# Performance work log

Measured on AMD Instinct MI355X. Metric: run time of the kernel, lower is better.

The kernel has to match this reference:

```python
import jax, jax.numpy as jnp
import numpy as np

B, P, ED, AD, DD, E, V, T = 64, 196, 2048, 512, 512, 300, 1000, 96


def setup_inputs() -> dict:
    key = jax.random.key(0)
    ks = jax.random.split(key, 24)
    s = 0.02  # small init scale for weights
    lens = jax.random.randint(ks[2], (B,), 2, T + 1).astype(jnp.int32)
    lens = lens.at[0].set(T)  # ensure max(decode_lengths) == T-1 (static)
    return {
        'encoder_out': jax.random.normal(ks[0], (B, P, ED), jnp.float32),
        'encoded_captions': jax.random.randint(ks[1], (B, T), 0, V),
        'caption_lengths': lens,
        'emb': jax.random.uniform(ks[3], (V, E), jnp.float32, -0.1, 0.1),
        'W_enc_att': jax.random.normal(ks[4], (ED, AD), jnp.float32) * s,
        'b_enc_att': jnp.zeros((AD,), jnp.float32),
        'W_dec_att': jax.random.normal(ks[5], (DD, AD), jnp.float32) * s,
        'b_dec_att': jnp.zeros((AD,), jnp.float32),
        'w_full': jax.random.normal(ks[6], (AD,), jnp.float32) * s,
        'b_full': jnp.zeros((), jnp.float32),
        'W_init_h': jax.random.normal(ks[7], (ED, DD), jnp.float32) * s,
        'b_init_h': jnp.zeros((DD,), jnp.float32),
        'W_init_c': jax.random.normal(ks[8], (ED, DD), jnp.float32) * s,
        'b_init_c': jnp.zeros((DD,), jnp.float32),
        'W_fbeta': jax.random.normal(ks[9], (DD, ED), jnp.float32) * s,
        'b_fbeta': jnp.zeros((ED,), jnp.float32),
        'W_ih': jax.random.normal(ks[10], (E + ED, 4 * DD), jnp.float32) * s,
        'b_ih': jnp.zeros((4 * DD,), jnp.float32),
        'W_hh': jax.random.normal(ks[11], (DD, 4 * DD), jnp.float32) * s,
        'b_hh': jnp.zeros((4 * DD,), jnp.float32),
        'W_fc': jax.random.uniform(ks[12], (DD, V), jnp.float32, -0.1, 0.1),
        'b_fc': jnp.zeros((V,), jnp.float32),
    }


def reference(encoder_out, encoded_captions, caption_lengths, emb,
              W_enc_att, b_enc_att, W_dec_att, b_dec_att, w_full, b_full,
              W_init_h, b_init_h, W_init_c, b_init_c, W_fbeta, b_fbeta,
              W_ih, b_ih, W_hh, b_hh, W_fc, b_fc):
    # Sort by caption length, descending (stable like torch.sort on ints)
    sort_ind = jnp.argsort(-caption_lengths)
    lens = caption_lengths[sort_ind]
    eo = encoder_out[sort_ind]                  # [B,P,ED]
    caps = encoded_captions[sort_ind]           # [B,T]
    decode_lengths = lens - 1                   # [B]

    embs = emb[caps]                            # [B,T,E]
    mean_eo = eo.mean(axis=1)                   # [B,ED]
    h0 = mean_eo @ W_init_h + b_init_h          # [B,DD]
    c0 = mean_eo @ W_init_c + b_init_c

    # encoder-side attention projection is step-invariant: hoist it
    att1 = eo @ W_enc_att + b_enc_att           # [B,P,AD]

    Tdec = T - 1
    ts = jnp.arange(Tdec)
    masks = (decode_lengths[None, :] > ts[:, None]).astype(eo.dtype)  # [Tdec,B]
    emb_seq = jnp.swapaxes(embs[:, :Tdec, :], 0, 1)                    # [Tdec,B,E]

    def step(carry, xs):
        h, c = carry
        emb_t, m = xs                           # [B,E], [B]
        mb = m[:, None]
        # Bahdanau attention
        att2 = h @ W_dec_att + b_dec_att        # [B,AD]
        e = jnp.einsum('bpa,a->bp', jax.nn.relu(att1 + att2[:, None, :]), w_full) + b_full
        alpha = jax.nn.softmax(e, axis=1)       # [B,P]
        awe = jnp.einsum('bpd,bp->bd', eo, alpha)  # [B,ED]
        gate = jax.nn.sigmoid(h @ W_fbeta + b_fbeta)
        x = jnp.concatenate([emb_t, gate * awe], axis=1)  # [B,E+ED]
        # LSTMCell (torch gate order: i, f, g, o)
        gates = x @ W_ih + b_ih + h @ W_hh + b_hh
        i, f, g, o = jnp.split(gates, 4, axis=1)
        c_new = jax.nn.sigmoid(f) * c + jax.nn.sigmoid(i) * jnp.tanh(g)
        h_new = jax.nn.sigmoid(o) * jnp.tanh(c_new)
        # only active rows (sorted so they are a prefix) update state
        h2 = mb * h_new + (1.0 - mb) * h
        c2 = mb * c_new + (1.0 - mb) * c
        preds = (h2 @ W_fc + b_fc) * mb         # dropout = identity (eval)
        return (h2, c2), (preds, alpha * mb)

    (_, _), (preds, alphas) = jax.lax.scan(step, (h0, c0), (emb_seq, masks))
    predictions = jnp.swapaxes(preds, 0, 1)     # [B,Tdec,V]
    alphas = jnp.swapaxes(alphas, 0, 1)         # [B,Tdec,P]
    return predictions, caps, decode_lengths, alphas, sort_ind
```

## Files before the change

### kernel.cpp

```cpp
#include <hip/hip_runtime.h>
#include <stddef.h>
#include <math.h>

static constexpr int B = 64, P = 196, ED = 2048, AD = 512, DD = 512, E = 300, V = 1000, T = 96, TD = 95;
static constexpr int KX = E + ED;
static constexpr int KTOT = KX + DD;
static constexpr int KSPLIT = 8;
static constexpr int KPER = 368;
static constexpr int NG = 4 * DD;

static constexpr size_t POFF   = 0;
static constexpr size_t CAPOFF = (size_t)B * TD * V;
static constexpr size_t DLOFF  = CAPOFF + (size_t)B * T;
static constexpr size_t AOFF   = DLOFF + B;
static constexpr size_t SOFF   = AOFF + (size_t)B * TD * P;

__device__ __forceinline__ float sigm(float x) { return 1.0f / (1.0f + expf(-x)); }

__global__ __launch_bounds__(64) void k_sort(const int* __restrict__ lens,
                                             const int* __restrict__ caps_in,
                                             int* __restrict__ sidx,
                                             int* __restrict__ dlen,
                                             int* __restrict__ caps_s,
                                             unsigned int* __restrict__ cnt,
                                             float* __restrict__ out) {
    __shared__ int sl[B];
    __shared__ int ss[B];
    int i = threadIdx.x;
    sl[i] = lens[i];
    cnt[i] = 0u;
    __syncthreads();
    int li = sl[i];
    int r = 0;
    for (int j = 0; j < B; j++) {
        int lj = sl[j];
        r += (lj > li) || (lj == li && j < i);
    }
    ss[r] = i;
    sidx[r] = i;
    dlen[r] = li - 1;
    out[DLOFF + r] = (float)(li - 1);
    out[SOFF + r] = (float)i;
    __syncthreads();
    for (int idx = i; idx < B * T; idx += B) {
        int b = idx / T, tt = idx % T;
        int v = caps_in[ss[b] * T + tt];
        caps_s[idx] = v;
        out[CAPOFF + idx] = (float)v;
    }
}

__global__ __launch_bounds__(256) void k_emball(const float* __restrict__ emb,
                                                const int* __restrict__ caps_s,
                                                float* __restrict__ embT) {
    int t = blockIdx.x;
    int k0 = blockIdx.y * 60;
    for (int l = threadIdx.x; l < 60 * 64; l += 256) {
        int r = l >> 6, b = l & 63;
        int k = k0 + r;
        int cap = caps_s[b * T + t];
        embT[((size_t)t * E + k) * B + b] = emb[(size_t)cap * E + k];
    }
}

__global__ __launch_bounds__(256) void k_mean(const float* __restrict__ eo,
                                              const int* __restrict__ sidx,
                                              float* __restrict__ mean_eo) {
    int b = blockIdx.y;
    int d = blockIdx.x * 256 + threadIdx.x;
    const float* base = eo + ((size_t)sidx[b] * P) * ED + d;
    float s = 0.f;
    for (int p = 0; p < P; p++) s += base[(size_t)p * ED];
    mean_eo[(size_t)b * ED + d] = s * (1.0f / (float)P);
}

__global__ __launch_bounds__(256) void k_init(const float* __restrict__ mean_eo,
                                              const float* __restrict__ Wh, const float* __restrict__ bh,
                                              const float* __restrict__ Wc, const float* __restrict__ bc,
                                              float* __restrict__ h0, float* __restrict__ c0,
                                              float* __restrict__ xT) {
    int idx = blockIdx.x * 256 + threadIdx.x;
    int b = idx >> 9, j = idx & 511;
    const float* m = mean_eo + (size_t)b * ED;
    float ah = bh[j], ac = bc[j];
    for (int k = 0; k < ED; k++) {
        float mv = m[k];
        ah += mv * Wh[(size_t)k * DD + j];
        ac += mv * Wc[(size_t)k * DD + j];
    }
    h0[idx] = ah;
    c0[idx] = ac;
    xT[(size_t)(KX + DD + j) * B + b] = ah;
}

__global__ __launch_bounds__(256) void k_att1(const float* __restrict__ eo,
                                              const float* __restrict__ W,
                                              const float* __restrict__ bias,
                                              const int* __restrict__ sidx,
                                              float* __restrict__ att1) {
    int m0 = blockIdx.x * 64, n0 = blockIdx.y * 64;
    __shared__ float sA[16][68];
    __shared__ float sB[16][68];
    int tid = threadIdx.x;
    int tx = tid & 15, ty = tid >> 4;
    float acc[4][4] = {};

    int la_m = tid >> 2;
    int la_k = (tid & 3) * 4;
    int lb_k = tid >> 4;
    int lb_n = (tid & 15) * 4;

    int mA = m0 + la_m;
    int bA = mA / P, pA = mA % P;
    const float* arow = eo + ((size_t)sidx[bA] * P + pA) * ED;

    for (int k0 = 0; k0 < ED; k0 += 16) {
        float4 av = *(const float4*)(arow + k0 + la_k);
        sA[la_k + 0][la_m] = av.x;
        sA[la_k + 1][la_m] = av.y;
        sA[la_k + 2][la_m] = av.z;
        sA[la_k + 3][la_m] = av.w;
        float4 bv = *(const float4*)(W + (size_t)(k0 + lb_k) * AD + n0 + lb_n);
        *(float4*)&sB[lb_k][lb_n] = bv;
        __syncthreads();
#pragma unroll
        for (int kk = 0; kk < 16; kk++) {
            float4 a4 = *(const float4*)&sA[kk][ty * 4];
            float4 b4 = *(const float4*)&sB[kk][tx * 4];
            float av_[4] = {a4.x, a4.y, a4.z, a4.w};
            float bv_[4] = {b4.x, b4.y, b4.z, b4.w};
#pragma unroll
            for (int i = 0; i < 4; i++)
#pragma unroll
                for (int j = 0; j < 4; j++) acc[i][j] += av_[i] * bv_[j];
        }
        __syncthreads();
    }
#pragma unroll
    for (int i = 0; i < 4; i++) {
        int m = m0 + ty * 4 + i;
        int n = n0 + tx * 4;
        float4 o;
        o.x = acc[i][0] + bias[n + 0];
        o.y = acc[i][1] + bias[n + 1];
        o.z = acc[i][2] + bias[n + 2];
        o.w = acc[i][3] + bias[n + 3];
        *(float4*)(att1 + (size_t)m * AD + n) = o;
    }
}

__global__ __launch_bounds__(256) void kA1(const float* __restrict__ hprev,
                                           const float* __restrict__ Wda, const float* __restrict__ bda,
                                           const float* __restrict__ Wfb, const float* __restrict__ bfb,
                                           float* __restrict__ att2g,
                                           float* __restrict__ fg) {
    int bx = blockIdx.x;
    int tid = threadIdx.x;
    int n0 = bx * 32;
    bool is_att = (n0 < AD);
    const float* W = is_att ? Wda : Wfb;
    int ld = is_att ? AD : ED;
    int colb = is_att ? n0 : n0 - AD;
    __shared__ float sH[2][16][68];
    __shared__ float sW[2][16][36];
    float acc[4][2] = {};
    int tb = tid & 15, tn = tid >> 4;
    int hb = tid >> 2, hq = tid & 3;
    int wk = tid >> 3, wn = (tid & 7) * 4;

    float4 hreg = *(const float4*)(hprev + (size_t)hb * DD + hq * 4);
    float4 wreg = make_float4(0.f, 0.f, 0.f, 0.f);
    if (tid < 128) wreg = *(const float4*)(W + (size_t)wk * ld + colb + wn);
    sH[0][hq * 4 + 0][hb] = hreg.x;
    sH[0][hq * 4 + 1][hb] = hreg.y;
    sH[0][hq * 4 + 2][hb] = hreg.z;
    sH[0][hq * 4 + 3][hb] = hreg.w;
    if (tid < 128) *(float4*)&sW[0][wk][wn] = wreg;
    __syncthreads();

    for (int tl = 0; tl < 32; tl++) {
        int cur = tl & 1, nxt = cur ^ 1;
        if (tl < 31) {
            int k0 = (tl + 1) * 16;
            hreg = *(const float4*)(hprev + (size_t)hb * DD + k0 + hq * 4);
            if (tid < 128) wreg = *(const float4*)(W + (size_t)(k0 + wk) * ld + colb + wn);
        }
#pragma unroll
        for (int kk = 0; kk < 16; kk++) {
            float4 hv = *(const float4*)&sH[cur][kk][tb * 4];
            float w0 = sW[cur][kk][tn * 2 + 0];
            float w1 = sW[cur][kk][tn * 2 + 1];
            acc[0][0] += hv.x * w0; acc[0][1] += hv.x * w1;
            acc[1][0] += hv.y * w0; acc[1][1] += hv.y * w1;
            acc[2][0] += hv.z * w0; acc[2][1] += hv.z * w1;
            acc[3][0] += hv.w * w0; acc[3][1] += hv.w * w1;
        }
        if (tl < 31) {
            sH[nxt][hq * 4 + 0][hb] = hreg.x;
            sH[nxt][hq * 4 + 1][hb] = hreg.y;
            sH[nxt][hq * 4 + 2][hb] = hreg.z;
            sH[nxt][hq * 4 + 3][hb] = hreg.w;
            if (tid < 128) *(float4*)&sW[nxt][wk][wn] = wreg;
        }
        __syncthreads();
    }
#pragma unroll
    for (int i = 0; i < 4; i++)
#pragma unroll
        for (int j = 0; j < 2; j++) {
            int b = tb * 4 + i;
            int n = n0 + tn * 2 + j;
            float v = acc[i][j];
            if (is_att) att2g[(size_t)b * AD + n] = v + bda[n];
            else {
                int d = n - AD;
                fg[(size_t)b * ED + d] = sigm(v + bfb[d]);
            }
        }
}

__global__ __launch_bounds__(1024) void kA2(const float* __restrict__ att2g,
                                            const float* __restrict__ att1,
                                            const float* __restrict__ wf,
                                            const float* __restrict__ bfv,
                                            const int* __restrict__ dlen,
                                            float* __restrict__ alpha,
                                            float* __restrict__ out, int t) {
    int b = blockIdx.x;
    int tid = threadIdx.x;
    __shared__ float sa2[AD];
    __shared__ float swf[AD];
    __shared__ float se[P];
    __shared__ float red[1024];

    if (tid < AD) {
        sa2[tid] = att2g[(size_t)b * AD + tid];
        swf[tid] = wf[tid];
    }
    __syncthreads();

    int w = tid >> 6, lane = tid & 63;
    float bf0 = bfv[0];
#pragma unroll 2
    for (int p = w; p < P; p += 16) {
        const float* row = att1 + ((size_t)b * P + p) * AD + lane * 8;
        float4 u0 = *(const float4*)row;
        float4 u1 = *(const float4*)(row + 4);
        float4 s0 = *(const float4*)&sa2[lane * 8];
        float4 s1 = *(const float4*)&sa2[lane * 8 + 4];
        float4 w0 = *(const float4*)&swf[lane * 8];
        float4 w1 = *(const float4*)&swf[lane * 8 + 4];
        float acc = fmaxf(u0.x + s0.x, 0.f) * w0.x + fmaxf(u0.y + s0.y, 0.f) * w0.y +
                    fmaxf(u0.z + s0.z, 0.f) * w0.z + fmaxf(u0.w + s0.w, 0.f) * w0.w +
                    fmaxf(u1.x + s1.x, 0.f) * w1.x + fmaxf(u1.y + s1.y, 0.f) * w1.y +
                    fmaxf(u1.z + s1.z, 0.f) * w1.z + fmaxf(u1.w + s1.w, 0.f) * w1.w;
#pragma unroll
        for (int m = 32; m >= 1; m >>= 1) acc += __shfl_xor(acc, m, 64);
        if (lane == 0) se[p] = acc + bf0;
    }
    __syncthreads();

    red[tid] = (tid < P) ? se[tid] : -1e30f;
    __syncthreads();
    for (int s = 512; s > 0; s >>= 1) {
        if (tid < s) red[tid] = fmaxf(red[tid], red[tid + s]);
        __syncthreads();
    }
    float mx = red[0];
    __syncthreads();
    float ex = (tid < P) ? expf(se[tid] - mx) : 0.f;
    red[tid] = ex;
    __syncthreads();
    for (int s = 512; s > 0; s >>= 1) {
        if (tid < s) red[tid] += red[tid + s];
        __syncthreads();
    }
    float inv = 1.0f / red[0];
    if (tid < P) {
        float a = ex * inv;
        alpha[(size_t)b * P + tid] = a;
        float m = (dlen[b] > t) ? 1.f : 0.f;
        out[AOFF + ((size_t)b * TD + t) * P + tid] = a * m;
    }
}

__global__ __launch_bounds__(256) void kB(const float* __restrict__ eo,
                                          const int* __restrict__ sidx,
                                          const float* __restrict__ alpha,
                                          const float* __restrict__ fg,
                                          float* __restrict__ xT) {
    int b = blockIdx.y, ch = blockIdx.x, tid = threadIdx.x;
    int pg = tid >> 6, lane = tid & 63;
    __shared__ float sal[P];
    __shared__ float part[4][260];
    if (tid < P) sal[tid] = alpha[(size_t)b * P + tid];
    __syncthreads();
    int d = ch * 256 + lane * 4;
    const float* base = eo + ((size_t)sidx[b] * P) * ED + d;
    float ax = 0.f, ay = 0.f, az = 0.f, aw = 0.f;
#pragma unroll 7
    for (int i = 0; i < 49; i++) {
        int p = pg + i * 4;
        float4 v = *(const float4*)(base + (size_t)p * ED);
        float a = sal[p];
        ax += v.x * a; ay += v.y * a; az += v.z * a; aw += v.w * a;
    }
    part[pg][lane * 4 + 0] = ax;
    part[pg][lane * 4 + 1] = ay;
    part[pg][lane * 4 + 2] = az;
    part[pg][lane * 4 + 3] = aw;
    __syncthreads();
    if (tid < 64) {
        int d0 = ch * 256 + tid * 4;
        float4 g = *(const float4*)(fg + (size_t)b * ED + d0);
        float s0 = part[0][tid * 4 + 0] + part[1][tid * 4 + 0] + part[2][tid * 4 + 0] + part[3][tid * 4 + 0];
        float s1 = part[0][tid * 4 + 1] + part[1][tid * 4 + 1] + part[2][tid * 4 + 1] + part[3][tid * 4 + 1];
        float s2 = part[0][tid * 4 + 2] + part[1][tid * 4 + 2] + part[2][tid * 4 + 2] + part[3][tid * 4 + 2];
        float s3 = part[0][tid * 4 + 3] + part[1][tid * 4 + 3] + part[2][tid * 4 + 3] + part[3][tid * 4 + 3];
        xT[(size_t)(E + d0 + 0) * B + b] = g.x * s0;
        xT[(size_t)(E + d0 + 1) * B + b] = g.y * s1;
        xT[(size_t)(E + d0 + 2) * B + b] = g.z * s2;
        xT[(size_t)(E + d0 + 3) * B + b] = g.w * s3;
    }
}

__global__ __launch_bounds__(256) void kCD(const float* __restrict__ xT,
                                           const float* __restrict__ embT_t,
                                           const float* __restrict__ xh_r,
                                           const float* __restrict__ Wih,
                                           const float* __restrict__ Whh,
                                           float* __restrict__ part,
                                           unsigned int* __restrict__ cnt,
                                           const float* __restrict__ bih,
                                           const float* __restrict__ bhh,
                                           const float* __restrict__ h0,
                                           float* __restrict__ hseq,
                                           const float* __restrict__ cread,
                                           float* __restrict__ cwrite,
                                           const int* __restrict__ dlen,
                                           float* __restrict__ xh_w, int t) {
    int bx = blockIdx.x;
    int ks = bx >> 6, nb = bx & 63;
    int n0 = nb * 32;
    int tid = threadIdx.x;
    int tb = tid & 15, tn = tid >> 4;
    int wk = tid >> 3, wn = (tid & 7) * 4;
    __shared__ float sW[2][16][36];
    __shared__ unsigned int sOld;
    float acc[4][2] = {};
    int kbase = ks * KPER;

    auto ldw = [&](int tile) -> float4 {
        int kg = kbase + tile * 16 + wk;
        float4 wv = make_float4(0.f, 0.f, 0.f, 0.f);
        if (kg < KX) wv = *(const float4*)&Wih[(size_t)kg * NG + n0 + wn];
        else if (kg < KTOT) wv = *(const float4*)&Whh[(size_t)(kg - KX) * NG + n0 + wn];
        return wv;
    };

    float4 wreg = make_float4(0.f, 0.f, 0.f, 0.f);
    if (tid < 128) {
        wreg = ldw(0);
        *(float4*)&sW[0][wk][wn] = wreg;
    }
    __syncthreads();

    for (int tile = 0; tile < 23; tile++) {
        int cur = tile & 1, nxt = cur ^ 1;
        if (tile < 22 && tid < 128) wreg = ldw(tile + 1);
#pragma unroll
        for (int kk = 0; kk < 16; kk++) {
            int kg = kbase + tile * 16 + kk;
            float4 xv = make_float4(0.f, 0.f, 0.f, 0.f);
            if (kg < E) xv = *(const float4*)&embT_t[(size_t)kg * B + tb * 4];
            else if (kg < KX) xv = *(const float4*)&xT[(size_t)kg * B + tb * 4];
            else if (kg < KTOT) xv = *(const float4*)&xh_r[(size_t)(kg - KX) * B + tb * 4];
            float w0 = sW[cur][kk][tn * 2 + 0];
            float w1 = sW[cur][kk][tn * 2 + 1];
            acc[0][0] += xv.x * w0; acc[0][1] += xv.x * w1;
            acc[1][0] += xv.y * w0; acc[1][1] += xv.y * w1;
            acc[2][0] += xv.z * w0; acc[2][1] += xv.z * w1;
            acc[3][0] += xv.w * w0; acc[3][1] += xv.w * w1;
        }
        if (tile < 22 && tid < 128) *(float4*)&sW[nxt][wk][wn] = wreg;
        __syncthreads();
    }

#pragma unroll
    for (int i = 0; i < 4; i++)
#pragma unroll
        for (int j = 0; j < 2; j++) {
            int b = tb * 4 + i, lc = tn * 2 + j;
            __hip_atomic_store(&part[((size_t)ks * B + b) * NG + n0 + lc], acc[i][j],
                               __ATOMIC_RELAXED, __HIP_MEMORY_SCOPE_AGENT);
        }
    __syncthreads();
    int jg = nb & 15;
    if (tid == 0)
        sOld = __hip_atomic_fetch_add(&cnt[jg], 1u, __ATOMIC_ACQ_REL, __HIP_MEMORY_SCOPE_AGENT);
    __syncthreads();
    if (sOld != 31u) return;

    if (tid == 0)
        __hip_atomic_store(&cnt[jg], 0u, __ATOMIC_RELAXED, __HIP_MEMORY_SCOPE_AGENT);

    const float* holds = (t == 0) ? h0 : (hseq + (size_t)(t - 1) * B * DD);
#pragma unroll
    for (int rep = 0; rep < 8; rep++) {
        int idx = rep * 256 + tid;
        int bb = idx >> 5;
        int jj = idx & 31;
        int j = jg * 32 + jj;
        float g4[4];
#pragma unroll
        for (int g = 0; g < 4; g++) {
            float gv = bih[g * DD + j] + bhh[g * DD + j];
#pragma unroll
            for (int s = 0; s < KSPLIT; s++)
                gv += __hip_atomic_load(&part[((size_t)s * B + bb) * NG + g * 512 + j],
                                        __ATOMIC_RELAXED, __HIP_MEMORY_SCOPE_AGENT);
            g4[g] = gv;
        }
        float cold = cread[(size_t)bb * DD + j];
        float hold = holds[(size_t)bb * DD + j];
        float cnew = sigm(g4[1]) * cold + sigm(g4[0]) * tanhf(g4[2]);
        float hnew = sigm(g4[3]) * tanhf(cnew);
        bool m = dlen[bb] > t;
        float h2 = m ? hnew : hold;
        float c2 = m ? cnew : cold;
        hseq[(size_t)t * B * DD + (size_t)bb * DD + j] = h2;
        cwrite[(size_t)bb * DD + j] = c2;
        xh_w[(size_t)j * B + bb] = h2;
    }
}

__global__ __launch_bounds__(256) void k_predsall(const float* __restrict__ hseq,
                                                  const float* __restrict__ Wfc,
                                                  const float* __restrict__ bfc,
                                                  const int* __restrict__ dlen,
                                                  float* __restrict__ out) {
    int t = blockIdx.x;
    int n0 = blockIdx.y * 64;
    int tid = threadIdx.x;
    int tx = tid & 15, ty = tid >> 4;
    __shared__ float sA[16][68];
    __shared__ float sB[16][68];
    float acc[4][4] = {};
    const float* A = hseq + (size_t)t * B * DD;

    for (int k0 = 0; k0 < DD; k0 += 16) {
        {
            int b = tid >> 2, q = tid & 3;
            float4 hv = *(const float4*)(A + (size_t)b * DD + k0 + q * 4);
            sA[q * 4 + 0][b] = hv.x;
            sA[q * 4 + 1][b] = hv.y;
            sA[q * 4 + 2][b] = hv.z;
            sA[q * 4 + 3][b] = hv.w;
        }
        {
            int kk = tid >> 4, nn = (tid & 15) * 4;
            int c = n0 + nn;
            const float* wrow = Wfc + (size_t)(k0 + kk) * V;
            float4 wv;
            if (c + 3 < V) wv = *(const float4*)(wrow + c);
            else {
                wv.x = (c + 0 < V) ? wrow[c + 0] : 0.f;
                wv.y = (c + 1 < V) ? wrow[c + 1] : 0.f;
                wv.z = (c + 2 < V) ? wrow[c + 2] : 0.f;
                wv.w = (c + 3 < V) ? wrow[c + 3] : 0.f;
            }
            *(float4*)&sB[kk][nn] = wv;
        }
        __syncthreads();
#pragma unroll
        for (int kk = 0; kk < 16; kk++) {
            float4 a4 = *(const float4*)&sA[kk][ty * 4];
            float4 b4 = *(const float4*)&sB[kk][tx * 4];
            float av_[4] = {a4.x, a4.y, a4.z, a4.w};
            float bv_[4] = {b4.x, b4.y, b4.z, b4.w};
#pragma unroll
            for (int i = 0; i < 4; i++)
#pragma unroll
                for (int j = 0; j < 4; j++) acc[i][j] += av_[i] * bv_[j];
        }
        __syncthreads();
    }
#pragma unroll
    for (int i = 0; i < 4; i++) {
        int b = ty * 4 + i;
        bool m = dlen[b] > t;
#pragma unroll
        for (int j = 0; j < 4; j++) {
            int n = n0 + tx * 4 + j;
            if (n < V)
                out[POFF + ((size_t)b * TD + t) * V + n] = m ? (acc[i][j] + bfc[n]) : 0.f;
        }
    }
}

extern "C" void kernel_launch(void* const* d_in, const int* in_sizes, int n_in,
                              void* d_out, int out_size, void* d_ws, size_t ws_size,
                              hipStream_t stream) {
    const float* eo    = (const float*)d_in[0];
    const int*   caps  = (const int*)d_in[1];
    const int*   lens  = (const int*)d_in[2];
    const float* emb   = (const float*)d_in[3];
    const float* Wea   = (const float*)d_in[4];
    const float* bea   = (const float*)d_in[5];
    const float* Wda   = (const float*)d_in[6];
    const float* bda   = (const float*)d_in[7];
    const float* wfull = (const float*)d_in[8];
    const float* bfull = (const float*)d_in[9];
    const float* Wih_  = (const float*)d_in[10];
    const float* bih_  = (const float*)d_in[11];
    const float* Wic   = (const float*)d_in[12];
    const float* bic   = (const float*)d_in[13];
    const float* Wfb   = (const float*)d_in[14];
    const float* bfb   = (const float*)d_in[15];
    const float* Wih   = (const float*)d_in[16];
    const float* bih   = (const float*)d_in[17];
    const float* Whh   = (const float*)d_in[18];
    const float* bhh   = (const float*)d_in[19];
    const float* Wfc   = (const float*)d_in[20];
    const float* bfc   = (const float*)d_in[21];
    float* out = (float*)d_out;

    char* w = (char*)d_ws;
    auto carve = [&](size_t bytes) -> void* {
        void* p = (void*)w;
        w += (bytes + 255) & ~(size_t)255;
        return p;
    };
    int* sidx      = (int*)carve(B * 4);
    int* dlen      = (int*)carve(B * 4);
    int* caps_s    = (int*)carve((size_t)B * T * 4);
    unsigned int* cnt = (unsigned int*)carve(64 * 4);
    float* mean_eo = (float*)carve((size_t)B * ED * 4);
    float* h0      = (float*)carve((size_t)B * DD * 4);
    float* cb0     = (float*)carve((size_t)B * DD * 4);
    float* cb1     = (float*)carve((size_t)B * DD * 4);
    float* att1    = (float*)carve((size_t)B * P * AD * 4);
    float* alphaW  = (float*)carve((size_t)B * P * 4);
    float* att2g   = (float*)carve((size_t)B * AD * 4);
    float* fg      = (float*)carve((size_t)B * ED * 4);
    float* xT      = (float*)carve((size_t)(KTOT + DD) * B * 4);
    float* part    = (float*)carve((size_t)KSPLIT * B * NG * 4);
    float* hseq    = (float*)carve((size_t)TD * B * DD * 4);
    float* embT    = (float*)carve((size_t)TD * E * B * 4);
    float* cb[2] = {cb0, cb1};

    k_sort<<<1, 64, 0, stream>>>(lens, caps, sidx, dlen, caps_s, cnt, out);
    k_emball<<<dim3(TD, 5), 256, 0, stream>>>(emb, caps_s, embT);
    k_mean<<<dim3(ED / 256, B), 256, 0, stream>>>(eo, sidx, mean_eo);
    k_init<<<(B * DD) / 256, 256, 0, stream>>>(mean_eo, Wih_, bih_, Wic, bic, h0, cb1, xT);
    k_att1<<<dim3((B * P) / 64, AD / 64), 256, 0, stream>>>(eo, Wea, bea, sidx, att1);

    for (int t = 0; t < TD; t++) {
        const float* hprev = (t == 0) ? h0 : (hseq + (size_t)(t - 1) * B * DD);
        kA1<<<80, 256, 0, stream>>>(hprev, Wda, bda, Wfb, bfb, att2g, fg);
        kA2<<<64, 1024, 0, stream>>>(att2g, att1, wfull, bfull, dlen, alphaW, out, t);
        kB<<<dim3(8, B), 256, 0, stream>>>(eo, sidx, alphaW, fg, xT);
        const float* xh_r = xT + (size_t)(KX + ((t + 1) & 1) * DD) * B;
        float*       xh_w = xT + (size_t)(KX + (t & 1) * DD) * B;
        kCD<<<512, 256, 0, stream>>>(xT, embT + (size_t)t * E * B, xh_r, Wih, Whh, part, cnt,
                                     bih, bhh, h0, hseq, cb[(t + 1) & 1], cb[t & 1], dlen, xh_w, t);
    }
    k_predsall<<<dim3(TD, 16), 256, 0, stream>>>(hseq, Wfc, bfc, dlen, out);
}
```

Baseline: 17.27 ms.

## Split-K the per-step h projections and spread attention scoring across more blocks

The per-step kernel that projects h into att2 and the f_beta gate now splits its K dimension four ways, running 320 blocks instead of 80. A per-column-tile atomic counter lets the last block sum the partials and apply the bias or sigmoid. The attention-score kernel is split into 256 smaller blocks that only write raw scores. Softmax and the alpha output move into the weighted-sum kernel, where each of the 8 channel chunks recomputes the softmax redundantly. The aim is more parallelism in latency-bound per-timestep kernels, at the cost of extra partial-sum traffic, atomics and duplicated softmax work.

```diff
diff --git a/kernel.cpp b/kernel.cpp
--- a/kernel.cpp
+++ b/kernel.cpp
@@ -8,6 +8,7 @@
 static constexpr int KSPLIT = 8;
 static constexpr int KPER = 368;
 static constexpr int NG = 4 * DD;
+static constexpr int NC = 2560;
 
 static constexpr size_t POFF   = 0;
 static constexpr size_t CAPOFF = (size_t)B * TD * V;
@@ -29,6 +30,7 @@
     int i = threadIdx.x;
     sl[i] = lens[i];
     cnt[i] = 0u;
+    cnt[i + 64] = 0u;
     __syncthreads();
     int li = sl[i];
     int r = 0;
@@ -150,27 +152,34 @@
 }
 
 __global__ __launch_bounds__(256) void kA1(const float* __restrict__ hprev,
-                                           const float* __restrict__ Wda, const float* __restrict__ bda,
-                                           const float* __restrict__ Wfb, const float* __restrict__ bfb,
+                                           const float* __restrict__ Wda,
+                                           const float* __restrict__ Wfb,
+                                           const float* __restrict__ bda,
+                                           const float* __restrict__ bfb,
+                                           float* __restrict__ part1,
+                                           unsigned int* __restrict__ cnt1,
                                            float* __restrict__ att2g,
                                            float* __restrict__ fg) {
     int bx = blockIdx.x;
-    int tid = threadIdx.x;
-    int n0 = bx * 32;
+    int nb = bx >> 2, ks = bx & 3;
+    int n0 = nb * 32;
     bool is_att = (n0 < AD);
     const float* W = is_att ? Wda : Wfb;
     int ld = is_att ? AD : ED;
     int colb = is_att ? n0 : n0 - AD;
+    int kbase = ks * 128;
+    int tid = threadIdx.x;
     __shared__ float sH[2][16][68];
     __shared__ float sW[2][16][36];
+    __shared__ unsigned int sOld;
     float acc[4][2] = {};
     int tb = tid & 15, tn = tid >> 4;
     int hb = tid >> 2, hq = tid & 3;
     int wk = tid >> 3, wn = (tid & 7) * 4;
 
-    float4 hreg = *(const float4*)(hprev + (size_t)hb * DD + hq * 4);
+    float4 hreg = *(const float4*)(hprev + (size_t)hb * DD + kbase + hq * 4);
     float4 wreg = make_float4(0.f, 0.f, 0.f, 0.f);
-    if (tid < 128) wreg = *(const float4*)(W + (size_t)wk * ld + colb + wn);
+    if (tid < 128) wreg = *(const float4*)(W + (size_t)(kbase + wk) * ld + colb + wn);
     sH[0][hq * 4 + 0][hb] = hreg.x;
     sH[0][hq * 4 + 1][hb] = hreg.y;
     sH[0][hq * 4 + 2][hb] = hreg.z;
@@ -178,10 +187,10 @@
     if (tid < 128) *(float4*)&sW[0][wk][wn] = wreg;
     __syncthreads();
 
-    for (int tl = 0; tl < 32; tl++) {
+    for (int tl = 0; tl < 8; tl++) {
         int cur = tl & 1, nxt = cur ^ 1;
-        if (tl < 31) {
-            int k0 = (tl + 1) * 16;
+        if (tl < 7) {
+            int k0 = kbase + (tl + 1) * 16;
             hreg = *(const float4*)(hprev + (size_t)hb * DD + k0 + hq * 4);
             if (tid < 128) wreg = *(const float4*)(W + (size_t)(k0 + wk) * ld + colb + wn);
         }
@@ -195,7 +204,7 @@
             acc[2][0] += hv.z * w0; acc[2][1] += hv.z * w1;
             acc[3][0] += hv.w * w0; acc[3][1] += hv.w * w1;
         }
-        if (tl < 31) {
+        if (tl < 7) {
             sH[nxt][hq * 4 + 0][hb] = hreg.x;
             sH[nxt][hq * 4 + 1][hb] = hreg.y;
             sH[nxt][hq * 4 + 2][hb] = hreg.z;
@@ -204,45 +213,61 @@
         }
         __syncthreads();
     }
+
 #pragma unroll
     for (int i = 0; i < 4; i++)
 #pragma unroll
         for (int j = 0; j < 2; j++) {
-            int b = tb * 4 + i;
-            int n = n0 + tn * 2 + j;
-            float v = acc[i][j];
-            if (is_att) att2g[(size_t)b * AD + n] = v + bda[n];
-            else {
-                int d = n - AD;
-                fg[(size_t)b * ED + d] = sigm(v + bfb[d]);
-            }
-        }
-}
-
-__global__ __launch_bounds__(1024) void kA2(const float* __restrict__ att2g,
+            int b = tb * 4 + i, n = n0 + tn * 2 + j;
+            __hip_atomic_store(&part1[((size_t)ks * B + b) * NC + n], acc[i][j],
+                               __ATOMIC_RELAXED, __HIP_MEMORY_SCOPE_AGENT);
+        }
+    __syncthreads();
+    if (tid == 0)
+        sOld = __hip_atomic_fetch_add(&cnt1[nb], 1u, __ATOMIC_ACQ_REL, __HIP_MEMORY_SCOPE_AGENT);
+    __syncthreads();
+    if (sOld != 3u) return;
+
+    if (tid == 0)
+        __hip_atomic_store(&cnt1[nb], 0u, __ATOMIC_RELAXED, __HIP_MEMORY_SCOPE_AGENT);
+#pragma unroll
+    for (int rep = 0; rep < 8; rep++) {
+        int idx = rep * 256 + tid;
+        int b = idx >> 5, nn = idx & 31;
+        int n = n0 + nn;
+        float s = 0.f;
+#pragma unroll
+        for (int k = 0; k < 4; k++)
+            s += __hip_atomic_load(&part1[((size_t)k * B + b) * NC + n],
+                                   __ATOMIC_RELAXED, __HIP_MEMORY_SCOPE_AGENT);
+        if (is_att) att2g[(size_t)b * AD + n] = s + bda[n];
+        else {
+            int d = n - AD;
+            fg[(size_t)b * ED + d] = sigm(s + bfb[d]);
+        }
+    }
+}
+
+__global__ __launch_bounds__(256) void kA2e(const float* __restrict__ att2g,
                                             const float* __restrict__ att1,
                                             const float* __restrict__ wf,
                                             const float* __restrict__ bfv,
-                                            const int* __restrict__ dlen,
-                                            float* __restrict__ alpha,
-                                            float* __restrict__ out, int t) {
-    int b = blockIdx.x;
+                                            float* __restrict__ eW) {
+    int bid = blockIdx.x;
+    int b = bid >> 2, ch = bid & 3;
     int tid = threadIdx.x;
     __shared__ float sa2[AD];
     __shared__ float swf[AD];
-    __shared__ float se[P];
-    __shared__ float red[1024];
-
-    if (tid < AD) {
-        sa2[tid] = att2g[(size_t)b * AD + tid];
-        swf[tid] = wf[tid];
-    }
+    sa2[tid] = att2g[(size_t)b * AD + tid];
+    sa2[tid + 256] = att2g[(size_t)b * AD + tid + 256];
+    swf[tid] = wf[tid];
+    swf[tid + 256] = wf[tid + 256];
     __syncthreads();
 
     int w = tid >> 6, lane = tid & 63;
     float bf0 = bfv[0];
-#pragma unroll 2
-    for (int p = w; p < P; p += 16) {
+    for (int pl = w; pl < 49; pl += 4) {
+        int p = ch * 49 + pl;
         const float* row = att1 + ((size_t)b * P + p) * AD + lane * 8;
         float4 u0 = *(const float4*)row;
         float4 u1 = *(const float4*)(row + 4);
@@ -255,14 +280,29 @@
                     fmaxf(u1.x + s1.x, 0.f) * w1.x + fmaxf(u1.y + s1.y, 0.f) * w1.y +
                     fmaxf(u1.z + s1.z, 0.f) * w1.z + fmaxf(u1.w + s1.w, 0.f) * w1.w;
 #pragma unroll
-        for (int m = 32; m >= 1; m >>= 1) acc += __shfl_xor(acc, m, 64);
-        if (lane == 0) se[p] = acc + bf0;
-    }
-    __syncthreads();
-
-    red[tid] = (tid < P) ? se[tid] : -1e30f;
-    __syncthreads();
-    for (int s = 512; s > 0; s >>= 1) {
+        for (int mm = 32; mm >= 1; mm >>= 1) acc += __shfl_xor(acc, mm, 64);
+        if (lane == 0) eW[(size_t)b * P + p] = acc + bf0;
+    }
+}
+
+__global__ __launch_bounds__(256) void kB(const float* __restrict__ eo,
+                                          const int* __restrict__ sidx,
+                                          const float* __restrict__ eW,
+                                          const float* __restrict__ fg,
+                                          const int* __restrict__ dlen,
+                                          float* __restrict__ xT,
+                                          float* __restrict__ out, int t) {
+    int b = blockIdx.y, ch = blockIdx.x, tid = threadIdx.x;
+    __shared__ float se[256];
+    __shared__ float red[256];
+    __shared__ float sal[P];
+    __shared__ float part[4][260];
+
+    se[tid] = (tid < P) ? eW[(size_t)b * P + tid] : -1e30f;
+    __syncthreads();
+    red[tid] = se[tid];
+    __syncthreads();
+    for (int s = 128; s > 0; s >>= 1) {
         if (tid < s) red[tid] = fmaxf(red[tid], red[tid + s]);
         __syncthreads();
     }
@@ -271,30 +311,22 @@
     float ex = (tid < P) ? expf(se[tid] - mx) : 0.f;
     red[tid] = ex;
     __syncthreads();
-    for (int s = 512; s > 0; s >>= 1) {
+    for (int s = 128; s > 0; s >>= 1) {
         if (tid < s) red[tid] += red[tid + s];
         __syncthreads();
     }
     float inv = 1.0f / red[0];
     if (tid < P) {
         float a = ex * inv;
-        alpha[(size_t)b * P + tid] = a;
-        float m = (dlen[b] > t) ? 1.f : 0.f;
-        out[AOFF + ((size_t)b * TD + t) * P + tid] = a * m;
-    }
-}
-
-__global__ __launch_bounds__(256) void kB(const float* __restrict__ eo,
-                                          const int* __restrict__ sidx,
-                                          const float* __restrict__ alpha,
-                                          const float* __restrict__ fg,
-                                          float* __restrict__ xT) {
-    int b = blockIdx.y, ch = blockIdx.x, tid = threadIdx.x;
+        sal[tid] = a;
+        if (ch == 0) {
+            float m = (dlen[b] > t) ? 1.f : 0.f;
+            out[AOFF + ((size_t)b * TD + t) * P + tid] = a * m;
+        }
+    }
+    __syncthreads();
+
     int pg = tid >> 6, lane = tid & 63;
-    __shared__ float sal[P];
-    __shared__ float part[4][260];
-    if (tid < P) sal[tid] = alpha[(size_t)b * P + tid];
-    __syncthreads();
     int d = ch * 256 + lane * 4;
     const float* base = eo + ((size_t)sidx[b] * P) * ED + d;
     float ax = 0.f, ay = 0.f, az = 0.f, aw = 0.f;
@@ -330,7 +362,7 @@
                                            const float* __restrict__ Wih,
                                            const float* __restrict__ Whh,
                                            float* __restrict__ part,
-                                           unsigned int* __restrict__ cnt,
+                                           unsigned int* __restrict__ cntCD,
                                            const float* __restrict__ bih,
                                            const float* __restrict__ bhh,
                                            const float* __restrict__ h0,
@@ -397,12 +429,12 @@
     __syncthreads();
     int jg = nb & 15;
     if (tid == 0)
-        sOld = __hip_atomic_fetch_add(&cnt[jg], 1u, __ATOMIC_ACQ_REL, __HIP_MEMORY_SCOPE_AGENT);
+        sOld = __hip_atomic_fetch_add(&cntCD[jg], 1u, __ATOMIC_ACQ_REL, __HIP_MEMORY_SCOPE_AGENT);
     __syncthreads();
     if (sOld != 31u) return;
 
     if (tid == 0)
-        __hip_atomic_store(&cnt[jg], 0u, __ATOMIC_RELAXED, __HIP_MEMORY_SCOPE_AGENT);
+        __hip_atomic_store(&cntCD[jg], 0u, __ATOMIC_RELAXED, __HIP_MEMORY_SCOPE_AGENT);
 
     const float* holds = (t == 0) ? h0 : (hseq + (size_t)(t - 1) * B * DD);
 #pragma unroll
@@ -534,20 +566,23 @@
     int* sidx      = (int*)carve(B * 4);
     int* dlen      = (int*)carve(B * 4);
     int* caps_s    = (int*)carve((size_t)B * T * 4);
-    unsigned int* cnt = (unsigned int*)carve(64 * 4);
+    unsigned int* cnt = (unsigned int*)carve(128 * 4);
     float* mean_eo = (float*)carve((size_t)B * ED * 4);
     float* h0      = (float*)carve((size_t)B * DD * 4);
     float* cb0     = (float*)carve((size_t)B * DD * 4);
     float* cb1     = (float*)carve((size_t)B * DD * 4);
     float* att1    = (float*)carve((size_t)B * P * AD * 4);
-    float* alphaW  = (float*)carve((size_t)B * P * 4);
+    float* eWb     = (float*)carve((size_t)B * P * 4);
     float* att2g   = (float*)carve((size_t)B * AD * 4);
     float* fg      = (float*)carve((size_t)B * ED * 4);
     float* xT      = (float*)carve((size_t)(KTOT + DD) * B * 4);
     float* part    = (float*)carve((size_t)KSPLIT * B * NG * 4);
+    float* part1   = (float*)carve((size_t)4 * B * NC * 4);
     float* hseq    = (float*)carve((size_t)TD * B * DD * 4);
     float* embT    = (float*)carve((size_t)TD * E * B * 4);
     float* cb[2] = {cb0, cb1};
+    unsigned int* cnt1  = cnt;
+    unsigned int* cntCD = cnt + 96;
 
     k_sort<<<1, 64, 0, stream>>>(lens, caps, sidx, dlen, caps_s, cnt, out);
     k_emball<<<dim3(TD, 5), 256, 0, stream>>>(emb, caps_s, embT);
@@ -557,12 +592,12 @@
 
     for (int t = 0; t < TD; t++) {
         const float* hprev = (t == 0) ? h0 : (hseq + (size_t)(t - 1) * B * DD);
-        kA1<<<80, 256, 0, stream>>>(hprev, Wda, bda, Wfb, bfb, att2g, fg);
-        kA2<<<64, 1024, 0, stream>>>(att2g, att1, wfull, bfull, dlen, alphaW, out, t);
-        kB<<<dim3(8, B), 256, 0, stream>>>(eo, sidx, alphaW, fg, xT);
+        kA1<<<320, 256, 0, stream>>>(hprev, Wda, Wfb, bda, bfb, part1, cnt1, att2g, fg);
+        kA2e<<<256, 256, 0, stream>>>(att2g, att1, wfull, bfull, eWb);
+        kB<<<dim3(8, B), 256, 0, stream>>>(eo, sidx, eWb, fg, dlen, xT, out, t);
         const float* xh_r = xT + (size_t)(KX + ((t + 1) & 1) * DD) * B;
         float*       xh_w = xT + (size_t)(KX + (t & 1) * DD) * B;
-        kCD<<<512, 256, 0, stream>>>(xT, embT + (size_t)t * E * B, xh_r, Wih, Whh, part, cnt,
+        kCD<<<512, 256, 0, stream>>>(xT, embT + (size_t)t * E * B, xh_r, Wih, Whh, part, cntCD,
                                      bih, bhh, h0, hseq, cb[(t + 1) & 1], cb[t & 1], dlen, xh_w, t);
     }
     k_predsall<<<dim3(TD, 16), 256, 0, stream>>>(hseq, Wfc, bfc, dlen, out);
```

New measurement: 16.87 ms. 2.3% less time.
